# Optimization experiments

Measured on AMD Instinct MI355X. Metric: run time of the kernel, lower is better.

## Reference

```python
import jax, jax.numpy as jnp
import numpy as np

B, C, T, H = 32, 256, 512, 8
EPS = 1e-5
NEG_INF = jnp.float32(-1e9)


def setup_inputs() -> dict:
    key = jax.random.key(0)
    ks = jax.random.split(key, 10)
    inp = {
        "seq": jax.random.normal(ks[0], (B, C, T), dtype=jnp.float32),
        "mask": jax.random.randint(ks[1], (B, T), 0, 2, dtype=jnp.int32),
        "Wq": jax.random.normal(ks[2], (C, C), dtype=jnp.float32) * 0.05,
        "bq": jnp.zeros((C,), dtype=jnp.float32),
        "Wk": jax.random.normal(ks[3], (C, C), dtype=jnp.float32) * 0.05,
        "bk": jnp.zeros((C,), dtype=jnp.float32),
        "Wv": jax.random.normal(ks[4], (C, C), dtype=jnp.float32) * 0.05,
        "bv": jnp.zeros((C,), dtype=jnp.float32),
        "gamma": jnp.ones((C,), dtype=jnp.float32),
        "beta": jnp.zeros((C,), dtype=jnp.float32),
    }
    return inp


def reference(seq, mask, Wq, bq, Wk, bk, Wv, bv, gamma, beta):
    d = C // H  # per-head dim
    s = jnp.transpose(seq, (0, 2, 1))  # [B, T, C]
    # ReLU'd projections (torch Linear: x @ W.T + b)
    Q = jax.nn.relu(s @ Wq.T + bq)
    K = jax.nn.relu(s @ Wk.T + bk)
    V = jax.nn.relu(s @ Wv.T + bv)
    # head split: channel block h -> head h (torch cat(split, dim=0) order = h*B+b)
    Qh = Q.reshape(B, T, H, d).transpose(2, 0, 1, 3)  # [H, B, T, d]
    Kh = K.reshape(B, T, H, d).transpose(2, 0, 1, 3)
    Vh = V.reshape(B, T, H, d).transpose(2, 0, 1, 3)
    scores = jnp.einsum('hbtd,hbsd->hbts', Qh, Kh) / jnp.sqrt(jnp.float32(d))
    # additive key mask before softmax
    key_mask = (mask == 0)[None, :, None, :]  # [1, B, 1, T]
    scores = jnp.where(key_mask, NEG_INF, scores)
    # multiplicative query mask after softmax
    qmask = mask.astype(jnp.float32)[None, :, :, None]  # [1, B, T, 1]
    att = jax.nn.softmax(scores, axis=-1) * qmask
    # dropout with keep_prob=1.0 is identity
    o = jnp.einsum('hbts,hbsd->hbtd', att, Vh)  # [H, B, T, d]
    x = o.transpose(1, 2, 0, 3).reshape(B, T, C)  # heads concatenated on channels
    x = jnp.transpose(x, (0, 2, 1))  # [B, C, T]
    # BatchNorm(pre_mask=True, post_mask=is_mask=True), training-mode batch stats
    m = (mask == 1)[:, None, :]  # [B, 1, T]
    x = jnp.where(m, x, jnp.float32(0.0))
    mean = jnp.mean(x, axis=(0, 2))
    var = jnp.mean((x - mean[None, :, None]) ** 2, axis=(0, 2))  # biased var (torch BN)
    xn = (x - mean[None, :, None]) * jax.lax.rsqrt(var + EPS)[None, :, None]
    x = gamma[None, :, None] * xn + beta[None, :, None]
    x = jnp.where(m, x, jnp.float32(0.0))
    return x
```

## Files before the change

kernel.cpp:

```cpp
#include <hip/hip_runtime.h>
#include <math.h>

#define NB 32
#define NC 256
#define NT 512
#define NH 8
#define ND 32
#define SCALE 0.17677669529663687f
#define LOG2E 1.4426950408889634f
#define QSCALE (SCALE * LOG2E)
#define DEFER_THR 8.0f

typedef __attribute__((ext_vector_type(8))) __bf16 bf16x8;
typedef __attribute__((ext_vector_type(4))) __bf16 bf16x4;
typedef __attribute__((ext_vector_type(4))) float  f32x4;

static __device__ __forceinline__ f32x4 mfma16x16x32(bf16x8 a, bf16x8 b, f32x4 c) {
    return __builtin_amdgcn_mfma_f32_16x16x32_bf16(a, b, c, 0, 0, 0);
}

__global__ __launch_bounds__(256) void qkv_mfma(
    const float* __restrict__ seq, const int* __restrict__ mask,
    const float* __restrict__ Wq, const float* __restrict__ bq,
    const float* __restrict__ Wk, const float* __restrict__ bk,
    const float* __restrict__ Wv, const float* __restrict__ bv,
    __bf16* __restrict__ Qh, __bf16* __restrict__ Kh, __bf16* __restrict__ VhT,
    float* __restrict__ stats)
{
    __shared__ __bf16 As[64][264];
    __shared__ __bf16 Ws[3][64][40];

    const int tid = threadIdx.x;
    const int t0  = blockIdx.x * 64;
    const int co0 = blockIdx.y * 64;
    const int bb  = blockIdx.z;

    if (blockIdx.x == 0 && blockIdx.y == 0 && bb == 0 && tid < 128)
        ((float4*)stats)[tid] = make_float4(0.f, 0.f, 0.f, 0.f);

    {
        const int cl = tid & 15;
        const int t4 = (tid >> 4) * 4;
        for (int it = 0; it < 16; ++it) {
            const int c = it*16 + cl;
            const float4 v = *(const float4*)&seq[((size_t)(bb*NC + c))*NT + t0 + t4];
            As[t4+0][c] = (__bf16)v.x;
            As[t4+1][c] = (__bf16)v.y;
            As[t4+2][c] = (__bf16)v.z;
            As[t4+3][c] = (__bf16)v.w;
        }
    }

    const float* Wp[3] = {Wq, Wk, Wv};

    f32x4 acc[3][4];
    #pragma unroll
    for (int p = 0; p < 3; ++p)
        #pragma unroll
        for (int n = 0; n < 4; ++n) acc[p][n] = (f32x4)0.f;

    const int l   = tid & 63;
    const int w   = tid >> 6;
    const int lr  = l & 15;
    const int lk8 = (l >> 4) * 8;

    int wp_[6], wco[6], wc4[6];
    #pragma unroll
    for (int i = 0; i < 6; ++i) {
        const int lin = i*256 + tid;
        wp_[i] = lin >> 9;
        const int r = lin & 511;
        wco[i] = r >> 3;
        wc4[i] = (r & 7) * 4;
    }

    float4 wreg[6];
    #pragma unroll
    for (int i = 0; i < 6; ++i)
        wreg[i] = *(const float4*)&Wp[wp_[i]][(size_t)(co0 + wco[i])*NC + wc4[i]];

    for (int kc = 0; kc < 8; ++kc) {
        __syncthreads();
        #pragma unroll
        for (int i = 0; i < 6; ++i) {
            bf16x4 wb;
            wb[0] = (__bf16)wreg[i].x; wb[1] = (__bf16)wreg[i].y;
            wb[2] = (__bf16)wreg[i].z; wb[3] = (__bf16)wreg[i].w;
            *(bf16x4*)&Ws[wp_[i]][wco[i]][wc4[i]] = wb;
        }
        __syncthreads();

        if (kc < 7) {
            #pragma unroll
            for (int i = 0; i < 6; ++i)
                wreg[i] = *(const float4*)&Wp[wp_[i]][(size_t)(co0 + wco[i])*NC + (kc+1)*32 + wc4[i]];
        }

        const bf16x8 a = *(const bf16x8*)&As[w*16 + lr][kc*32 + lk8];
        #pragma unroll
        for (int p = 0; p < 3; ++p)
            #pragma unroll
            for (int n = 0; n < 4; ++n) {
                const bf16x8 bfr = *(const bf16x8*)&Ws[p][n*16 + lr][lk8];
                acc[p][n] = mfma16x16x32(a, bfr, acc[p][n]);
            }
    }

    const int tba = t0 + w*16 + (l>>4)*4;

    {
        const float* bias2[2] = {bq, bk};
        __bf16* outp2[2] = {Qh, Kh};
        #pragma unroll
        for (int p = 0; p < 2; ++p) {
            #pragma unroll
            for (int n = 0; n < 4; ++n) {
                const int c  = co0 + n*16 + lr;
                const int hh = c >> 5, jj = c & 31;
                const float bv_ = bias2[p][c];
                const float sc  = (p == 0) ? QSCALE : 1.f;
                __bf16* op = outp2[p] + ((size_t)(bb*NH + hh)*NT)*ND + jj;
                #pragma unroll
                for (int r = 0; r < 4; ++r)
                    op[(size_t)(tba + r)*ND] = (__bf16)(fmaxf(acc[p][n][r] + bv_, 0.f) * sc);
            }
        }
    }

    {
        float km[4];
        #pragma unroll
        for (int r = 0; r < 4; ++r)
            km[r] = (mask[bb*NT + tba + r] != 0) ? 1.f : 0.f;
        #pragma unroll
        for (int n = 0; n < 4; ++n) {
            const int c  = co0 + n*16 + lr;
            const int hh = c >> 5, jj = c & 31;
            const float bv_ = bv[c];
            bf16x4 vv;
            #pragma unroll
            for (int r = 0; r < 4; ++r)
                vv[r] = (__bf16)(fmaxf(acc[2][n][r] + bv_, 0.f) * km[r]);
            *(bf16x4*)&VhT[((size_t)(bb*NH + hh)*ND + jj)*NT + tba] = vv;
        }
    }
}

__global__ __launch_bounds__(256) void attn_mfma(
    const __bf16* __restrict__ Qh, const __bf16* __restrict__ Kh,
    const __bf16* __restrict__ VhT, const int* __restrict__ mask,
    float* __restrict__ xout, float* __restrict__ stats)
{
    __shared__ __bf16 Ks[64][40];
    __shared__ __bf16 VTs[33*64];
    __shared__ __bf16 PA[128*64];
    __shared__ float  bnsum[32][4];
    __shared__ float  bnsum2[32][4];

    const int tid = threadIdx.x;
    const int t0  = blockIdx.x * 128;
    const int h   = blockIdx.y;
    const int bb  = blockIdx.z;
    const int bh  = bb*NH + h;
    const __bf16* Qp = Qh  + (size_t)bh*NT*ND;
    const __bf16* Kp = Kh  + (size_t)bh*NT*ND;
    const __bf16* Vp = VhT + (size_t)bh*ND*NT;

    const int l   = tid & 63;
    const int w   = tid >> 6;
    const int lr  = l & 15;
    const int g   = l >> 4;
    const int swz = (lr & 7) << 3;

    bf16x8 qb[2];
    #pragma unroll
    for (int ct = 0; ct < 2; ++ct)
        qb[ct] = *(const bf16x8*)&Qp[(size_t)(t0 + w*32 + ct*16 + lr)*ND + g*8];

    f32x4 accO[2][2];
    f32x4 accL[2];
    #pragma unroll
    for (int jt = 0; jt < 2; ++jt)
        #pragma unroll
        for (int ct = 0; ct < 2; ++ct) accO[jt][ct] = (f32x4)0.f;
    accL[0] = (f32x4)0.f; accL[1] = (f32x4)0.f;
    float m_run[2] = {-1e30f, -1e30f};

    const int kv_s = tid >> 2, kv_c8 = (tid & 3) * 8;
    const int vt_j = tid >> 3, vt_s8 = (tid & 7) * 8;

    uint4 kreg = *(const uint4*)&Kp[(size_t)kv_s*ND + kv_c8];
    uint4 vreg = *(const uint4*)&Vp[(size_t)vt_j*NT + vt_s8];
    int   mreg = (tid < 64) ? mask[bb*NT + tid] : 0;

    for (int s0 = 0; s0 < NT; s0 += 64) {
        __syncthreads();
        *(uint4*)&Ks[kv_s][kv_c8] = kreg;
        *(uint4*)&VTs[vt_j*64 + (vt_s8 ^ ((vt_j & 7) << 3))] = vreg;
        if (tid < 64) VTs[32*64 + tid] = (__bf16)(mreg ? 1.f : 0.f);
        __syncthreads();

        if (s0 + 64 < NT) {
            const int sn = s0 + 64;
            kreg = *(const uint4*)&Kp[(size_t)(sn + kv_s)*ND + kv_c8];
            vreg = *(const uint4*)&Vp[(size_t)vt_j*NT + sn + vt_s8];
            if (tid < 64) mreg = mask[bb*NT + sn + tid];
        }

        bf16x8 kA[4];
        #pragma unroll
        for (int st = 0; st < 4; ++st)
            kA[st] = *(const bf16x8*)&Ks[st*16 + lr][g*8];
        f32x4 sst[2][4];
        __builtin_amdgcn_s_setprio(1);
        #pragma unroll
        for (int ct = 0; ct < 2; ++ct)
            #pragma unroll
            for (int st = 0; st < 4; ++st)
                sst[ct][st] = mfma16x16x32(kA[st], qb[ct], (f32x4)0.f);
        __builtin_amdgcn_s_setprio(0);

        #pragma unroll
        for (int ct = 0; ct < 2; ++ct) {
            float mx = -1e30f;
            #pragma unroll
            for (int st = 0; st < 4; ++st)
                #pragma unroll
                for (int r = 0; r < 4; ++r) mx = fmaxf(mx, sst[ct][st][r]);
            mx = fmaxf(mx, __shfl_xor(mx, 16));
            mx = fmaxf(mx, __shfl_xor(mx, 32));

            if (!__all(mx <= m_run[ct] + DEFER_THR)) {
                const float m_new = fmaxf(m_run[ct], mx);
                const float f = exp2f(m_run[ct] - m_new);
                #pragma unroll
                for (int jt = 0; jt < 2; ++jt)
                    #pragma unroll
                    for (int r = 0; r < 4; ++r) accO[jt][ct][r] *= f;
                #pragma unroll
                for (int r = 0; r < 4; ++r) accL[ct][r] *= f;
                m_run[ct] = m_new;
            }

            const int trow = w*32 + ct*16 + lr;
            #pragma unroll
            for (int st = 0; st < 4; ++st) {
                bf16x4 pb4;
                #pragma unroll
                for (int r = 0; r < 4; ++r)
                    pb4[r] = (__bf16)exp2f(sst[ct][st][r] - m_run[ct]);
                *(bf16x4*)&PA[trow*64 + ((st*16 + g*4) ^ swz)] = pb4;
            }
        }

        __builtin_amdgcn_s_setprio(1);
        #pragma unroll
        for (int kh = 0; kh < 2; ++kh) {
            const int co = (kh*32 + g*8);
            bf16x8 va[2], pb[2];
            #pragma unroll
            for (int jt = 0; jt < 2; ++jt)
                va[jt] = *(const bf16x8*)&VTs[(jt*16 + lr)*64 + (co ^ swz)];
            const bf16x8 vam = *(const bf16x8*)&VTs[32*64 + co];
            #pragma unroll
            for (int ct = 0; ct < 2; ++ct)
                pb[ct] = *(const bf16x8*)&PA[(w*32 + ct*16 + lr)*64 + (co ^ swz)];
            #pragma unroll
            for (int jt = 0; jt < 2; ++jt)
                #pragma unroll
                for (int ct = 0; ct < 2; ++ct)
                    accO[jt][ct] = mfma16x16x32(va[jt], pb[ct], accO[jt][ct]);
            #pragma unroll
            for (int ct = 0; ct < 2; ++ct)
                accL[ct] = mfma16x16x32(vam, pb[ct], accL[ct]);
        }
        __builtin_amdgcn_s_setprio(0);
    }

    float psum[2][4], psq[2][4];
    #pragma unroll
    for (int jt = 0; jt < 2; ++jt)
        #pragma unroll
        for (int r = 0; r < 4; ++r) { psum[jt][r] = 0.f; psq[jt][r] = 0.f; }

    #pragma unroll
    for (int ct = 0; ct < 2; ++ct) {
        const int t = t0 + w*32 + ct*16 + lr;
        const float rl = mask[bb*NT + t] ? (1.f / accL[ct][0]) : 0.f;
        #pragma unroll
        for (int jt = 0; jt < 2; ++jt) {
            #pragma unroll
            for (int r = 0; r < 4; ++r) {
                const int c = h*ND + jt*16 + g*4 + r;
                const float o = accO[jt][ct][r] * rl;
                xout[((size_t)(bb*NC + c))*NT + t] = o;
                psum[jt][r] += o;
                psq[jt][r]  += o*o;
            }
        }
    }
    #pragma unroll
    for (int jt = 0; jt < 2; ++jt)
        #pragma unroll
        for (int r = 0; r < 4; ++r)
            #pragma unroll
            for (int off = 1; off < 16; off <<= 1) {
                psum[jt][r] += __shfl_xor(psum[jt][r], off);
                psq[jt][r]  += __shfl_xor(psq[jt][r],  off);
            }
    if (lr == 0) {
        #pragma unroll
        for (int jt = 0; jt < 2; ++jt)
            #pragma unroll
            for (int r = 0; r < 4; ++r) {
                bnsum [jt*16 + g*4 + r][w] = psum[jt][r];
                bnsum2[jt*16 + g*4 + r][w] = psq[jt][r];
            }
    }
    __syncthreads();
    if (tid < 32) {
        const float s  = bnsum [tid][0] + bnsum [tid][1] + bnsum [tid][2] + bnsum [tid][3];
        const float s2 = bnsum2[tid][0] + bnsum2[tid][1] + bnsum2[tid][2] + bnsum2[tid][3];
        atomicAdd(&stats[h*ND + tid], s);
        atomicAdd(&stats[NC + h*ND + tid], s2);
    }
}

__global__ __launch_bounds__(256) void bn_apply_kernel(
    float* __restrict__ x, const float* __restrict__ stats,
    const float* __restrict__ gamma, const float* __restrict__ beta,
    const int* __restrict__ mask)
{
    const int idx = blockIdx.x*256 + threadIdx.x;
    const int t4 = idx & 127;
    const int c  = (idx >> 7) & 255;
    const int bb = idx >> 15;
    float4 v = ((const float4*)x)[idx];
    const int4 mk = *(const int4*)&mask[bb*NT + t4*4];
    const float mean = stats[c] * (1.f/16384.f);
    const float var  = fmaxf(stats[NC + c]*(1.f/16384.f) - mean*mean, 0.f);
    const float rstd = rsqrtf(var + 1e-5f);
    const float g = gamma[c], be = beta[c];
    v.x = mk.x ? fmaf((v.x - mean)*rstd, g, be) : 0.f;
    v.y = mk.y ? fmaf((v.y - mean)*rstd, g, be) : 0.f;
    v.z = mk.z ? fmaf((v.z - mean)*rstd, g, be) : 0.f;
    v.w = mk.w ? fmaf((v.w - mean)*rstd, g, be) : 0.f;
    ((float4*)x)[idx] = v;
}

extern "C" void kernel_launch(void* const* d_in, const int* in_sizes, int n_in,
                              void* d_out, int out_size, void* d_ws, size_t ws_size,
                              hipStream_t stream)
{
    const float* seq   = (const float*)d_in[0];
    const int*   mask  = (const int*)  d_in[1];
    const float* Wq    = (const float*)d_in[2];
    const float* bq    = (const float*)d_in[3];
    const float* Wk    = (const float*)d_in[4];
    const float* bk    = (const float*)d_in[5];
    const float* Wv    = (const float*)d_in[6];
    const float* bv    = (const float*)d_in[7];
    const float* gamma = (const float*)d_in[8];
    const float* beta  = (const float*)d_in[9];
    float* out = (float*)d_out;

    const size_t perMat = (size_t)NB*NH*NT*ND;
    __bf16* Qh  = (__bf16*)d_ws;
    __bf16* Kh  = Qh + perMat;
    __bf16* VhT = Kh + perMat;
    float* stats = (float*)(VhT + perMat);

    qkv_mfma<<<dim3(NT/64, NC/64, NB), 256, 0, stream>>>(
        seq, mask, Wq, bq, Wk, bk, Wv, bv, Qh, Kh, VhT, stats);
    attn_mfma<<<dim3(NT/128, NH, NB), 256, 0, stream>>>(
        Qh, Kh, VhT, mask, out, stats);
    bn_apply_kernel<<<dim3((NB*NC*NT/4)/256), 256, 0, stream>>>(
        out, stats, gamma, beta, mask);
}
```

Measured before the change: 147.5 us.

## Pre-convert seq and weights to bf16, double-buffer weight tiles in QKV GEMM

Adds prep kernels that transpose seq to a bf16 [B,T,C] layout once and convert the Q/K/V weights to bf16 with the Q scale folded in. The QKV GEMM then loads bf16 A fragments directly from global memory, uses a 128-token tile with two token subtiles per wave, and double-buffers the weight tile in LDS so each step needs one barrier. This removes the repeated fp32 seq reads and conversions across output-channel blocks. The cost is two extra launches and a bf16 intermediate written to and read back from memory.

Result: slower. 151.9 us (+3.0%).

```diff
diff --git a/kernel.cpp b/kernel.cpp
--- a/kernel.cpp
+++ b/kernel.cpp
@@ -19,119 +19,148 @@
     return __builtin_amdgcn_mfma_f32_16x16x32_bf16(a, b, c, 0, 0, 0);
 }
 
-__global__ __launch_bounds__(256) void qkv_mfma(
-    const float* __restrict__ seq, const int* __restrict__ mask,
-    const float* __restrict__ Wq, const float* __restrict__ bq,
-    const float* __restrict__ Wk, const float* __restrict__ bk,
-    const float* __restrict__ Wv, const float* __restrict__ bv,
-    __bf16* __restrict__ Qh, __bf16* __restrict__ Kh, __bf16* __restrict__ VhT,
-    float* __restrict__ stats)
-{
-    __shared__ __bf16 As[64][264];
-    __shared__ __bf16 Ws[3][64][40];
-
+__global__ __launch_bounds__(256) void prep_seq(
+    const float* __restrict__ seq, __bf16* __restrict__ seqT)
+{
+    __shared__ __bf16 lds[64][264];
     const int tid = threadIdx.x;
     const int t0  = blockIdx.x * 64;
+    const int bb  = blockIdx.y;
+    #pragma unroll
+    for (int it = 0; it < 16; ++it) {
+        const int lin = it*256 + tid;
+        const int c = lin >> 4, t4 = (lin & 15) * 4;
+        const float4 v = *(const float4*)&seq[((size_t)(bb*NC + c))*NT + t0 + t4];
+        lds[t4+0][c] = (__bf16)v.x;
+        lds[t4+1][c] = (__bf16)v.y;
+        lds[t4+2][c] = (__bf16)v.z;
+        lds[t4+3][c] = (__bf16)v.w;
+    }
+    __syncthreads();
+    #pragma unroll
+    for (int it = 0; it < 8; ++it) {
+        const int lin = it*256 + tid;
+        const int row = lin >> 5, u = lin & 31;
+        *(uint4*)&seqT[((size_t)(bb*NT) + t0 + row)*NC + u*8] = *(const uint4*)&lds[row][u*8];
+    }
+}
+
+__global__ __launch_bounds__(256) void prep_w(
+    const float* __restrict__ Wq, const float* __restrict__ Wk,
+    const float* __restrict__ Wv, __bf16* __restrict__ Wb,
+    float* __restrict__ stats)
+{
+    const int tid = threadIdx.x;
+    if (blockIdx.x == 0 && tid < 128)
+        ((float4*)stats)[tid] = make_float4(0.f, 0.f, 0.f, 0.f);
+    const int lin = blockIdx.x*256 + tid;
+    const int p = lin >> 14;
+    const int r = lin & 16383;
+    const float* W = (p == 0) ? Wq : ((p == 1) ? Wk : Wv);
+    const float sc = (p == 0) ? QSCALE : 1.f;
+    const float4 v = *(const float4*)&W[(size_t)r*4];
+    bf16x4 o;
+    o[0] = (__bf16)(v.x*sc); o[1] = (__bf16)(v.y*sc);
+    o[2] = (__bf16)(v.z*sc); o[3] = (__bf16)(v.w*sc);
+    *(bf16x4*)&Wb[(size_t)p*65536 + (size_t)r*4] = o;
+}
+
+__global__ __launch_bounds__(256) void qkv_mfma(
+    const __bf16* __restrict__ seqT, const __bf16* __restrict__ Wb,
+    const float* __restrict__ bq, const float* __restrict__ bk,
+    const float* __restrict__ bv, const int* __restrict__ mask,
+    __bf16* __restrict__ Qh, __bf16* __restrict__ Kh, __bf16* __restrict__ VhT)
+{
+    __shared__ __bf16 Ws[2][3][64][40];
+
+    const int tid = threadIdx.x;
+    const int t0  = blockIdx.x * 128;
     const int co0 = blockIdx.y * 64;
     const int bb  = blockIdx.z;
-
-    if (blockIdx.x == 0 && blockIdx.y == 0 && bb == 0 && tid < 128)
-        ((float4*)stats)[tid] = make_float4(0.f, 0.f, 0.f, 0.f);
-
-    {
-        const int cl = tid & 15;
-        const int t4 = (tid >> 4) * 4;
-        for (int it = 0; it < 16; ++it) {
-            const int c = it*16 + cl;
-            const float4 v = *(const float4*)&seq[((size_t)(bb*NC + c))*NT + t0 + t4];
-            As[t4+0][c] = (__bf16)v.x;
-            As[t4+1][c] = (__bf16)v.y;
-            As[t4+2][c] = (__bf16)v.z;
-            As[t4+3][c] = (__bf16)v.w;
-        }
-    }
-
-    const float* Wp[3] = {Wq, Wk, Wv};
-
-    f32x4 acc[3][4];
+    const int l = tid & 63, w = tid >> 6, lr = l & 15, g = l >> 4;
+
+    const int s_co = tid >> 2, s_c8 = (tid & 3) * 8;
+    const __bf16* sp = seqT + ((size_t)(bb*NT) + t0 + w*32)*NC;
+
+    f32x4 acc[3][4][2];
     #pragma unroll
     for (int p = 0; p < 3; ++p)
         #pragma unroll
-        for (int n = 0; n < 4; ++n) acc[p][n] = (f32x4)0.f;
-
-    const int l   = tid & 63;
-    const int w   = tid >> 6;
-    const int lr  = l & 15;
-    const int lk8 = (l >> 4) * 8;
-
-    int wp_[6], wco[6], wc4[6];
-    #pragma unroll
-    for (int i = 0; i < 6; ++i) {
-        const int lin = i*256 + tid;
-        wp_[i] = lin >> 9;
-        const int r = lin & 511;
-        wco[i] = r >> 3;
-        wc4[i] = (r & 7) * 4;
-    }
-
-    float4 wreg[6];
-    #pragma unroll
-    for (int i = 0; i < 6; ++i)
-        wreg[i] = *(const float4*)&Wp[wp_[i]][(size_t)(co0 + wco[i])*NC + wc4[i]];
+        for (int n = 0; n < 4; ++n)
+            #pragma unroll
+            for (int ct = 0; ct < 2; ++ct) acc[p][n][ct] = (f32x4)0.f;
+
+    uint4 wreg[3];
+    #pragma unroll
+    for (int p = 0; p < 3; ++p)
+        wreg[p] = *(const uint4*)&Wb[((size_t)p*256 + co0 + s_co)*NC + s_c8];
+    #pragma unroll
+    for (int p = 0; p < 3; ++p)
+        *(uint4*)&Ws[0][p][s_co][s_c8] = wreg[p];
+    #pragma unroll
+    for (int p = 0; p < 3; ++p)
+        wreg[p] = *(const uint4*)&Wb[((size_t)p*256 + co0 + s_co)*NC + 32 + s_c8];
+
+    bf16x8 a[2];
+    #pragma unroll
+    for (int ct = 0; ct < 2; ++ct)
+        a[ct] = *(const bf16x8*)&sp[(ct*16 + lr)*NC + g*8];
 
     for (int kc = 0; kc < 8; ++kc) {
         __syncthreads();
-        #pragma unroll
-        for (int i = 0; i < 6; ++i) {
-            bf16x4 wb;
-            wb[0] = (__bf16)wreg[i].x; wb[1] = (__bf16)wreg[i].y;
-            wb[2] = (__bf16)wreg[i].z; wb[3] = (__bf16)wreg[i].w;
-            *(bf16x4*)&Ws[wp_[i]][wco[i]][wc4[i]] = wb;
-        }
-        __syncthreads();
-
         if (kc < 7) {
             #pragma unroll
-            for (int i = 0; i < 6; ++i)
-                wreg[i] = *(const float4*)&Wp[wp_[i]][(size_t)(co0 + wco[i])*NC + (kc+1)*32 + wc4[i]];
-        }
-
-        const bf16x8 a = *(const bf16x8*)&As[w*16 + lr][kc*32 + lk8];
-        #pragma unroll
-        for (int p = 0; p < 3; ++p)
-            #pragma unroll
-            for (int n = 0; n < 4; ++n) {
-                const bf16x8 bfr = *(const bf16x8*)&Ws[p][n*16 + lr][lk8];
-                acc[p][n] = mfma16x16x32(a, bfr, acc[p][n]);
-            }
-    }
-
-    const int tba = t0 + w*16 + (l>>4)*4;
-
-    {
-        const float* bias2[2] = {bq, bk};
-        __bf16* outp2[2] = {Qh, Kh};
+            for (int p = 0; p < 3; ++p)
+                *(uint4*)&Ws[(kc+1)&1][p][s_co][s_c8] = wreg[p];
+        }
+        if (kc < 6) {
+            #pragma unroll
+            for (int p = 0; p < 3; ++p)
+                wreg[p] = *(const uint4*)&Wb[((size_t)p*256 + co0 + s_co)*NC + (kc+2)*32 + s_c8];
+        }
+        bf16x8 a_nxt[2];
+        const int kn = (kc < 7) ? kc + 1 : 7;
+        #pragma unroll
+        for (int ct = 0; ct < 2; ++ct)
+            a_nxt[ct] = *(const bf16x8*)&sp[(ct*16 + lr)*NC + kn*32 + g*8];
+
+        __builtin_amdgcn_s_setprio(1);
+        #pragma unroll
+        for (int p = 0; p < 3; ++p) {
+            bf16x8 wf[4];
+            #pragma unroll
+            for (int n = 0; n < 4; ++n)
+                wf[n] = *(const bf16x8*)&Ws[kc&1][p][n*16 + lr][g*8];
+            #pragma unroll
+            for (int n = 0; n < 4; ++n)
+                #pragma unroll
+                for (int ct = 0; ct < 2; ++ct)
+                    acc[p][n][ct] = mfma16x16x32(a[ct], wf[n], acc[p][n][ct]);
+        }
+        __builtin_amdgcn_s_setprio(0);
+        a[0] = a_nxt[0]; a[1] = a_nxt[1];
+    }
+
+    #pragma unroll
+    for (int ct = 0; ct < 2; ++ct) {
+        const int tb = t0 + w*32 + ct*16 + g*4;
         #pragma unroll
         for (int p = 0; p < 2; ++p) {
             #pragma unroll
             for (int n = 0; n < 4; ++n) {
                 const int c  = co0 + n*16 + lr;
                 const int hh = c >> 5, jj = c & 31;
-                const float bv_ = bias2[p][c];
-                const float sc  = (p == 0) ? QSCALE : 1.f;
-                __bf16* op = outp2[p] + ((size_t)(bb*NH + hh)*NT)*ND + jj;
+                const float bv_ = (p == 0) ? bq[c]*QSCALE : bk[c];
+                __bf16* op = (p == 0 ? Qh : Kh) + ((size_t)(bb*NH + hh)*NT)*ND + jj;
                 #pragma unroll
                 for (int r = 0; r < 4; ++r)
-                    op[(size_t)(tba + r)*ND] = (__bf16)(fmaxf(acc[p][n][r] + bv_, 0.f) * sc);
-            }
-        }
-    }
-
-    {
+                    op[(size_t)(tb + r)*ND] = (__bf16)fmaxf(acc[p][n][ct][r] + bv_, 0.f);
+            }
+        }
         float km[4];
         #pragma unroll
         for (int r = 0; r < 4; ++r)
-            km[r] = (mask[bb*NT + tba + r] != 0) ? 1.f : 0.f;
+            km[r] = (mask[bb*NT + tb + r] != 0) ? 1.f : 0.f;
         #pragma unroll
         for (int n = 0; n < 4; ++n) {
             const int c  = co0 + n*16 + lr;
@@ -140,8 +169,8 @@
             bf16x4 vv;
             #pragma unroll
             for (int r = 0; r < 4; ++r)
-                vv[r] = (__bf16)(fmaxf(acc[2][n][r] + bv_, 0.f) * km[r]);
-            *(bf16x4*)&VhT[((size_t)(bb*NH + hh)*ND + jj)*NT + tba] = vv;
+                vv[r] = (__bf16)(fmaxf(acc[2][n][ct][r] + bv_, 0.f) * km[r]);
+            *(bf16x4*)&VhT[((size_t)(bb*NH + hh)*ND + jj)*NT + tb] = vv;
         }
     }
 }
@@ -365,13 +394,17 @@
     float* out = (float*)d_out;
 
     const size_t perMat = (size_t)NB*NH*NT*ND;
-    __bf16* Qh  = (__bf16*)d_ws;
-    __bf16* Kh  = Qh + perMat;
-    __bf16* VhT = Kh + perMat;
-    float* stats = (float*)(VhT + perMat);
-
-    qkv_mfma<<<dim3(NT/64, NC/64, NB), 256, 0, stream>>>(
-        seq, mask, Wq, bq, Wk, bk, Wv, bv, Qh, Kh, VhT, stats);
+    float*  stats = (float*)d_ws;
+    __bf16* Qh    = (__bf16*)((char*)d_ws + 4096);
+    __bf16* Kh    = Qh  + perMat;
+    __bf16* VhT   = Kh  + perMat;
+    __bf16* seqT  = VhT + perMat;
+    __bf16* Wb    = seqT + perMat;
+
+    prep_seq<<<dim3(NT/64, NB), 256, 0, stream>>>(seq, seqT);
+    prep_w<<<dim3(192), 256, 0, stream>>>(Wq, Wk, Wv, Wb, stats);
+    qkv_mfma<<<dim3(NT/128, NC/64, NB), 256, 0, stream>>>(
+        seqT, Wb, bq, bk, bv, mask, Qh, Kh, VhT);
     attn_mfma<<<dim3(NT/128, NH, NB), 256, 0, stream>>>(
         Qh, Kh, VhT, mask, out, stats);
     bn_apply_kernel<<<dim3((NB*NC*NT/4)/256), 256, 0, stream>>>(
```
